# Kernel tuning notes

Hardware: AMD Instinct MI355X
Metric: run time of the kernel (lower is better)

Reference implementation:

```python
import jax, jax.numpy as jnp
import numpy as np

B, C, H, W = 32, 256, 64, 64
HEADS, KDIM, VDIM = 8, 64, 64


def setup_inputs() -> dict:
    key = jax.random.key(0)
    ks = jax.random.split(key, 9)
    s = lambda fan: 1.0 / np.sqrt(fan)
    x = jax.random.normal(ks[0], (B, C, H, W), jnp.float32)
    Wq = jax.random.normal(ks[1], (KDIM * HEADS, C), jnp.float32) * s(C)
    bq = jnp.zeros((KDIM * HEADS,), jnp.float32)
    Wk = jax.random.normal(ks[2], (KDIM, C), jnp.float32) * s(C)
    bk = jnp.zeros((KDIM,), jnp.float32)
    Wv = jax.random.normal(ks[3], (VDIM, C), jnp.float32) * s(C)
    bv = jnp.zeros((VDIM,), jnp.float32)
    Wo = jax.random.normal(ks[4], (C, VDIM * HEADS), jnp.float32) * s(VDIM * HEADS)
    bo = jnp.zeros((C,), jnp.float32)
    return {"x": x, "Wq": Wq, "bq": bq, "Wk": Wk, "bk": bk,
            "Wv": Wv, "bv": bv, "Wo": Wo, "bo": bo}


def reference(x, Wq, bq, Wk, bk, Wv, bv, Wo, bo):
    b, c, h, w = x.shape
    n = h * w
    kd = Wk.shape[0]
    heads = Wq.shape[0] // kd
    xf = x.reshape(b, c, n)
    # 1x1 convs == channel matmuls
    q = jnp.einsum('oc,bcn->bon', Wq, xf) + bq[None, :, None]  # (b, heads*kd, n)
    k = jnp.einsum('oc,bcn->bon', Wk, xf) + bk[None, :, None]  # (b, kd, n)
    v = jnp.einsum('oc,bcn->bon', Wv, xf) + bv[None, :, None]  # (b, vd, n)
    q = q.reshape(b, heads, kd, n)
    q = jax.nn.softmax(q, axis=2)   # softmax over key_dim (dim=2 of bhdn)
    k = jax.nn.softmax(k, axis=2)   # softmax over n (dim=2 of bdn)
    ctx = jnp.einsum('bdn,ben->bde', k, v)          # (b, kd, vd)
    out = jnp.einsum('bhdn,bde->bhen', q, ctx)      # (b, heads, vd, n)
    out = out.reshape(b, heads * ctx.shape[2], n)
    out = jnp.einsum('oc,bcn->bon', Wo, out) + bo[None, :, None]
    return out.reshape(b, -1, h, w)
```

## Files before the change

kernel.cpp:

```cpp
#include <hip/hip_runtime.h>
#include <hip/hip_bf16.h>
#include <stdint.h>

#define BATCH 32
#define CDIM  256
#define NPIX  4096
#define HEADS 8
#define KD    64
#define VD    64
#define OQ    512

typedef __hip_bfloat16 bf16;
typedef __attribute__((ext_vector_type(8))) short bf16x8;
typedef __attribute__((ext_vector_type(4))) float floatx4;

union pack8 { bf16 h[8]; uint4 u; };

__device__ inline uint4 cvt8(const float* __restrict__ s) {
  float4 f0 = *reinterpret_cast<const float4*>(s);
  float4 f1 = *reinterpret_cast<const float4*>(s + 4);
  pack8 t;
  t.h[0] = __float2bfloat16(f0.x); t.h[1] = __float2bfloat16(f0.y);
  t.h[2] = __float2bfloat16(f0.z); t.h[3] = __float2bfloat16(f0.w);
  t.h[4] = __float2bfloat16(f1.x); t.h[5] = __float2bfloat16(f1.y);
  t.h[6] = __float2bfloat16(f1.z); t.h[7] = __float2bfloat16(f1.w);
  return t.u;
}

__global__ __launch_bounds__(256) void transpose_k(const float* __restrict__ x,
                                                   bf16* __restrict__ xT) {
  __shared__ bf16 t[64 * 72];
  const int tid = threadIdx.x;
  const int b = blockIdx.z;
  const int n0 = blockIdx.x * 64;
  const int c0 = blockIdx.y * 64;
  const float* xb = x + (size_t)b * CDIM * NPIX;
  for (int p = 0; p < 2; ++p) {
    int cl = p * 32 + (tid >> 3);
    int no = (tid & 7) * 8;
    *reinterpret_cast<uint4*>(&t[cl * 72 + no]) =
        cvt8(xb + (size_t)(c0 + cl) * NPIX + n0 + no);
  }
  __syncthreads();
  bf16* xTb = xT + (size_t)b * NPIX * CDIM;
  for (int p = 0; p < 2; ++p) {
    int nl = p * 32 + (tid >> 3);
    int co = (tid & 7) * 8;
    pack8 tmp;
    for (int j = 0; j < 8; ++j) tmp.h[j] = t[(co + j) * 72 + nl];
    *reinterpret_cast<uint4*>(xTb + (size_t)(n0 + nl) * CDIM + c0 + co) = tmp.u;
  }
}

__global__ __launch_bounds__(256, 2) void gemm_qkv(
    const bf16* __restrict__ xT,
    const float* __restrict__ Wq, const float* __restrict__ bq,
    const float* __restrict__ Wk, const float* __restrict__ bk,
    const float* __restrict__ Wv, const float* __restrict__ bv,
    bf16* __restrict__ qT, bf16* __restrict__ kT, bf16* __restrict__ vT) {
  __shared__ bf16 lsA[128 * 72];
  __shared__ bf16 lsB[128 * 72];
  const int tid = threadIdx.x;
  const int b  = blockIdx.z;
  const int bm = blockIdx.x;
  const int ot = blockIdx.y;
  const int lane = tid & 63;
  const int w    = tid >> 6;
  const int wm = w & 1, wn = w >> 1;
  const int l15 = lane & 15, quad = lane >> 4;

  const bf16* Ab = xT + (size_t)b * NPIX * CDIM + (size_t)bm * 128 * CDIM;

  floatx4 acc[4][4];
  const floatx4 zf = {0.f, 0.f, 0.f, 0.f};
  for (int i = 0; i < 4; ++i)
    for (int j = 0; j < 4; ++j) acc[i][j] = zf;

  for (int kb = 0; kb < CDIM / 64; ++kb) {
    __syncthreads();
    for (int ci = tid; ci < 1024; ci += 256) {
      int row = ci >> 3, off = (ci & 7) << 3;
      uint4 v = *reinterpret_cast<const uint4*>(Ab + (size_t)row * CDIM + kb * 64 + off);
      *reinterpret_cast<uint4*>(&lsA[row * 72 + off]) = v;
    }
    for (int ci = tid; ci < 1024; ci += 256) {
      int row = ci >> 3, off = (ci & 7) << 3;
      int o = ot * 128 + row;
      const float* src = (o < 512) ? (Wq + (size_t)o * CDIM)
                        : (o < 576) ? (Wk + (size_t)(o - 512) * CDIM)
                                    : (Wv + (size_t)(o - 576) * CDIM);
      *reinterpret_cast<uint4*>(&lsB[row * 72 + off]) = cvt8(src + kb * 64 + off);
    }
    __syncthreads();
    for (int kk = 0; kk < 64; kk += 32) {
      bf16x8 af[4], bfr[4];
      for (int mi = 0; mi < 4; ++mi)
        af[mi] = *reinterpret_cast<const bf16x8*>(&lsA[(wm * 64 + mi * 16 + l15) * 72 + kk + quad * 8]);
      for (int ni = 0; ni < 4; ++ni)
        bfr[ni] = *reinterpret_cast<const bf16x8*>(&lsB[(wn * 64 + ni * 16 + l15) * 72 + kk + quad * 8]);
      for (int mi = 0; mi < 4; ++mi)
        for (int ni = 0; ni < 4; ++ni)
          acc[mi][ni] = __builtin_amdgcn_mfma_f32_16x16x32_bf16(af[mi], bfr[ni], acc[mi][ni], 0, 0, 0);
    }
  }
  __syncthreads();

  bf16* ep = ((w < 2) ? lsA : lsB) + (w & 1) * (64 * 72);
  const int obase = ot * 128 + wn * 64;

  if (obase < 512) {
    float bias[4];
    for (int ni = 0; ni < 4; ++ni) bias[ni] = bq[obase + ni * 16 + l15];
    for (int mi = 0; mi < 4; ++mi) {
      for (int r = 0; r < 4; ++r) {
        float v0 = acc[mi][0][r] + bias[0];
        float v1 = acc[mi][1][r] + bias[1];
        float v2 = acc[mi][2][r] + bias[2];
        float v3 = acc[mi][3][r] + bias[3];
        float m = fmaxf(fmaxf(v0, v1), fmaxf(v2, v3));
        for (int off = 1; off < 16; off <<= 1) m = fmaxf(m, __shfl_xor(m, off));
        float e0 = __expf(v0 - m), e1 = __expf(v1 - m);
        float e2 = __expf(v2 - m), e3 = __expf(v3 - m);
        float s = e0 + e1 + e2 + e3;
        for (int off = 1; off < 16; off <<= 1) s += __shfl_xor(s, off);
        float inv = 1.0f / s;
        int lr = mi * 16 + quad * 4 + r;
        ep[lr * 72 +  0 + l15] = __float2bfloat16(e0 * inv);
        ep[lr * 72 + 16 + l15] = __float2bfloat16(e1 * inv);
        ep[lr * 72 + 32 + l15] = __float2bfloat16(e2 * inv);
        ep[lr * 72 + 48 + l15] = __float2bfloat16(e3 * inv);
      }
    }
  } else {
    const float* bp = (wn == 0) ? bk : bv;
    float bias[4];
    for (int ni = 0; ni < 4; ++ni) bias[ni] = bp[ni * 16 + l15];
    for (int mi = 0; mi < 4; ++mi)
      for (int r = 0; r < 4; ++r) {
        int lr = mi * 16 + quad * 4 + r;
        for (int ni = 0; ni < 4; ++ni)
          ep[lr * 72 + ni * 16 + l15] = __float2bfloat16(acc[mi][ni][r] + bias[ni]);
      }
  }
  __syncthreads();

  bf16* dst; int rstride;
  const int row0 = bm * 128 + wm * 64;
  if (obase < 512)      { dst = qT + (size_t)b * NPIX * OQ + (size_t)row0 * OQ + obase; rstride = OQ; }
  else if (obase == 512){ dst = kT + (size_t)b * NPIX * KD + (size_t)row0 * KD;         rstride = KD; }
  else                  { dst = vT + (size_t)b * NPIX * VD + (size_t)row0 * VD;         rstride = VD; }
  for (int p = 0; p < 8; ++p) {
    int lr = (lane >> 3) + p * 8;
    int co = (lane & 7) * 8;
    uint4 v = *reinterpret_cast<const uint4*>(&ep[lr * 72 + co]);
    *reinterpret_cast<uint4*>(dst + (size_t)lr * rstride + co) = v;
  }
}

__global__ __launch_bounds__(256) void ctx_partial(const bf16* __restrict__ kT,
                                                   const bf16* __restrict__ vT,
                                                   float* __restrict__ ctxn,
                                                   float* __restrict__ dnm) {
  __shared__ float ek[16 * 68];
  __shared__ float vv[16 * 68];
  const int tid = threadIdx.x;
  const int b = blockIdx.y, ci = blockIdx.x;
  const int dg = tid >> 4, eg = tid & 15;
  float acc[4][4] = {};
  float dloc = 0.f;
  for (int nb = 0; nb < 16; ++nb) {
    const int n0 = ci * 256 + nb * 16;
    __syncthreads();
    if (tid < 128) {
      int r = tid >> 3, off = (tid & 7) * 8;
      const bf16* src = kT + (size_t)b * NPIX * KD + (size_t)(n0 + r) * KD + off;
      for (int j = 0; j < 8; ++j) ek[r * 68 + off + j] = __expf(__bfloat162float(src[j]));
    } else {
      int t2 = tid - 128;
      int r = t2 >> 3, off = (t2 & 7) * 8;
      const bf16* src = vT + (size_t)b * NPIX * VD + (size_t)(n0 + r) * VD + off;
      for (int j = 0; j < 8; ++j) vv[r * 68 + off + j] = __bfloat162float(src[j]);
    }
    __syncthreads();
    for (int nn = 0; nn < 16; ++nn) {
      float4 e4 = *reinterpret_cast<const float4*>(&ek[nn * 68 + dg * 4]);
      float4 v4 = *reinterpret_cast<const float4*>(&vv[nn * 68 + eg * 4]);
      acc[0][0] += e4.x * v4.x; acc[0][1] += e4.x * v4.y; acc[0][2] += e4.x * v4.z; acc[0][3] += e4.x * v4.w;
      acc[1][0] += e4.y * v4.x; acc[1][1] += e4.y * v4.y; acc[1][2] += e4.y * v4.z; acc[1][3] += e4.y * v4.w;
      acc[2][0] += e4.z * v4.x; acc[2][1] += e4.z * v4.y; acc[2][2] += e4.z * v4.z; acc[2][3] += e4.z * v4.w;
      acc[3][0] += e4.w * v4.x; acc[3][1] += e4.w * v4.y; acc[3][2] += e4.w * v4.z; acc[3][3] += e4.w * v4.w;
    }
    if (tid < 64) {
      for (int nn = 0; nn < 16; ++nn) dloc += ek[nn * 68 + tid];
    }
  }
  for (int i = 0; i < 4; ++i)
    for (int j = 0; j < 4; ++j)
      atomicAdd(&ctxn[(size_t)b * 4096 + (dg * 4 + i) * 64 + eg * 4 + j], acc[i][j]);
  if (tid < 64) atomicAdd(&dnm[b * 64 + tid], dloc);
}

__global__ __launch_bounds__(256) void mbuild(const float* __restrict__ ctxn,
                                              const float* __restrict__ dnm,
                                              const float* __restrict__ Wo,
                                              bf16* __restrict__ Mm) {
  __shared__ float cn[64 * 68];
  const int h = blockIdx.x, b = blockIdx.y, tid = threadIdx.x;
  for (int ii = tid; ii < 4096; ii += 256) {
    int d = ii >> 6;
    cn[d * 68 + (ii & 63)] = ctxn[(size_t)b * 4096 + ii] / dnm[b * 64 + d];
  }
  __syncthreads();
  const int c = tid;
  const float* wrow = Wo + (size_t)c * OQ + h * 64;
  float wv[64];
  for (int e = 0; e < 64; ++e) wv[e] = wrow[e];
  bf16* mrow = Mm + (size_t)b * CDIM * OQ + (size_t)c * OQ + h * 64;
  for (int d = 0; d < 64; ++d) {
    float a = 0.f;
    for (int e = 0; e < 64; ++e) a += wv[e] * cn[d * 68 + e];
    mrow[d] = __float2bfloat16(a);
  }
}

__global__ __launch_bounds__(256, 2) void gemm_out(
    const bf16* __restrict__ Mm, const bf16* __restrict__ qT,
    const float* __restrict__ bo, float* __restrict__ out) {
  __shared__ bf16 lsA[128 * 72];
  __shared__ bf16 lsB[128 * 72];
  const int tid = threadIdx.x;
  const int b  = blockIdx.z;
  const int cm = blockIdx.x;
  const int nt = blockIdx.y;
  const int lane = tid & 63;
  const int w    = tid >> 6;
  const int wm = w & 1, wn = w >> 1;
  const int l15 = lane & 15, quad = lane >> 4;

  const bf16* Ab = Mm + (size_t)b * CDIM * OQ + (size_t)cm * 128 * OQ;
  const bf16* Bb = qT + (size_t)b * NPIX * OQ + (size_t)nt * 128 * OQ;

  floatx4 acc[4][4];
  const floatx4 zf = {0.f, 0.f, 0.f, 0.f};
  for (int i = 0; i < 4; ++i)
    for (int j = 0; j < 4; ++j) acc[i][j] = zf;

  for (int kb = 0; kb < OQ / 64; ++kb) {
    __syncthreads();
    for (int ci = tid; ci < 1024; ci += 256) {
      int row = ci >> 3, off = (ci & 7) << 3;
      uint4 v = *reinterpret_cast<const uint4*>(Ab + (size_t)row * OQ + kb * 64 + off);
      *reinterpret_cast<uint4*>(&lsA[row * 72 + off]) = v;
    }
    for (int ci = tid; ci < 1024; ci += 256) {
      int row = ci >> 3, off = (ci & 7) << 3;
      uint4 v = *reinterpret_cast<const uint4*>(Bb + (size_t)row * OQ + kb * 64 + off);
      *reinterpret_cast<uint4*>(&lsB[row * 72 + off]) = v;
    }
    __syncthreads();
    for (int kk = 0; kk < 64; kk += 32) {
      bf16x8 af[4], bfr[4];
      for (int mi = 0; mi < 4; ++mi)
        af[mi] = *reinterpret_cast<const bf16x8*>(&lsA[(wm * 64 + mi * 16 + l15) * 72 + kk + quad * 8]);
      for (int ni = 0; ni < 4; ++ni)
        bfr[ni] = *reinterpret_cast<const bf16x8*>(&lsB[(wn * 64 + ni * 16 + l15) * 72 + kk + quad * 8]);
      for (int mi = 0; mi < 4; ++mi)
        for (int ni = 0; ni < 4; ++ni)
          acc[mi][ni] = __builtin_amdgcn_mfma_f32_16x16x32_bf16(af[mi], bfr[ni], acc[mi][ni], 0, 0, 0);
    }
  }

  const int row0 = cm * 128 + wm * 64;
  const int col0 = nt * 128 + wn * 64;
  float* outb = out + (size_t)b * CDIM * NPIX;
  for (int mi = 0; mi < 4; ++mi)
    for (int r = 0; r < 4; ++r) {
      int c = row0 + mi * 16 + quad * 4 + r;
      float bias = bo[c];
      float* orow = outb + (size_t)c * NPIX + col0;
      for (int ni = 0; ni < 4; ++ni)
        orow[ni * 16 + l15] = acc[mi][ni][r] + bias;
    }
}

extern "C" void kernel_launch(void* const* d_in, const int* in_sizes, int n_in,
                              void* d_out, int out_size, void* d_ws, size_t ws_size,
                              hipStream_t stream) {
  const float* x  = (const float*)d_in[0];
  const float* Wq = (const float*)d_in[1];
  const float* bq = (const float*)d_in[2];
  const float* Wk = (const float*)d_in[3];
  const float* bk = (const float*)d_in[4];
  const float* Wv = (const float*)d_in[5];
  const float* bv = (const float*)d_in[6];
  const float* Wo = (const float*)d_in[7];
  const float* bo = (const float*)d_in[8];
  float* out = (float*)d_out;

  const size_t pb_xT  = (size_t)NPIX * CDIM * 2;
  const size_t pb_qT  = (size_t)NPIX * OQ * 2;
  const size_t pb_kT  = (size_t)NPIX * KD * 2;
  const size_t pb_vT  = (size_t)NPIX * VD * 2;
  const size_t pb_ctx = (size_t)KD * VD * 4;
  const size_t pb_dnm = (size_t)KD * 4;
  const size_t pb_Mm  = (size_t)CDIM * OQ * 2;
  const size_t perB = pb_xT + pb_qT + pb_kT + pb_vT + pb_ctx + pb_dnm + pb_Mm;

  int CB = 32;
  while (CB > 1 && (size_t)CB * perB > ws_size) CB >>= 1;

  char* ws = (char*)d_ws;
  bf16*  xT   = (bf16*)ws;                                  ws += (size_t)CB * pb_xT;
  bf16*  qT   = (bf16*)ws;                                  ws += (size_t)CB * pb_qT;
  bf16*  kT   = (bf16*)ws;                                  ws += (size_t)CB * pb_kT;
  bf16*  vT   = (bf16*)ws;                                  ws += (size_t)CB * pb_vT;
  float* ctxn = (float*)ws;                                 ws += (size_t)CB * pb_ctx;
  float* dnm  = (float*)ws;                                 ws += (size_t)CB * pb_dnm;
  bf16*  Mm   = (bf16*)ws;

  for (int b0 = 0; b0 < BATCH; b0 += CB) {
    const float* x_c  = x   + (size_t)b0 * CDIM * NPIX;
    float*      out_c = out + (size_t)b0 * CDIM * NPIX;
    hipMemsetAsync(ctxn, 0, (size_t)CB * (pb_ctx + pb_dnm), stream);
    transpose_k<<<dim3(64, 4, CB), 256, 0, stream>>>(x_c, xT);
    gemm_qkv<<<dim3(32, 5, CB), 256, 0, stream>>>(xT, Wq, bq, Wk, bk, Wv, bv, qT, kT, vT);
    ctx_partial<<<dim3(16, CB), 256, 0, stream>>>(kT, vT, ctxn, dnm);
    mbuild<<<dim3(HEADS, CB), 256, 0, stream>>>(ctxn, dnm, Wo, Mm);
    gemm_out<<<dim3(2, 32, CB), 256, 0, stream>>>(Mm, qT, bo, out_c);
  }
}
```

Measured before the change: 533.5 us.

## Use direct global-to-LDS loads with XOR-swizzled tiles and pre-converted bf16 weights

Both MFMA GEMMs now stage their tiles with global_load_lds 16-byte transfers straight into LDS, in place of register round-trips. The padded layout is replaced by an unpadded one with an XOR swizzle to avoid bank conflicts. The QKV weights are converted to bf16 once, in a new prep kernel, instead of every block converting fp32 weights on each K-step. The swizzled layout adds index arithmetic and depends on the async LDS-load semantics being correct.

```diff
diff --git a/kernel.cpp b/kernel.cpp
--- a/kernel.cpp
+++ b/kernel.cpp
@@ -9,6 +9,7 @@
 #define KD    64
 #define VD    64
 #define OQ    512
+#define OTOT  640
 
 typedef __hip_bfloat16 bf16;
 typedef __attribute__((ext_vector_type(8))) short bf16x8;
@@ -25,6 +26,34 @@
   t.h[4] = __float2bfloat16(f1.x); t.h[5] = __float2bfloat16(f1.y);
   t.h[6] = __float2bfloat16(f1.z); t.h[7] = __float2bfloat16(f1.w);
   return t.u;
+}
+
+__device__ inline void gload16(const bf16* g, bf16* l) {
+  __builtin_amdgcn_global_load_lds(
+      (const __attribute__((address_space(1))) void*)(g),
+      (__attribute__((address_space(3))) void*)(l), 16, 0, 0);
+}
+
+__device__ inline bf16x8 lds_frag(const bf16* base, int row, int colbyte) {
+  int off = row * 128 + (colbyte ^ ((row & 7) << 4));
+  return *reinterpret_cast<const bf16x8*>(reinterpret_cast<const char*>(base) + off);
+}
+__device__ inline void ep_store(bf16* ep, int row, int colbyte, bf16 v) {
+  int off = row * 128 + (colbyte ^ ((row & 7) << 4));
+  *reinterpret_cast<bf16*>(reinterpret_cast<char*>(ep) + off) = v;
+}
+
+__global__ __launch_bounds__(256) void prep_w(const float* __restrict__ Wq,
+                                              const float* __restrict__ Wk,
+                                              const float* __restrict__ Wv,
+                                              bf16* __restrict__ Wb) {
+  int i = blockIdx.x * 256 + threadIdx.x;
+  int o = i >> 5;
+  int off = (i & 31) * 8;
+  const float* src = (o < OQ)      ? (Wq + (size_t)o * CDIM + off)
+                   : (o < OQ + KD) ? (Wk + (size_t)(o - OQ) * CDIM + off)
+                                   : (Wv + (size_t)(o - OQ - KD) * CDIM + off);
+  *reinterpret_cast<uint4*>(Wb + (size_t)o * CDIM + off) = cvt8(src);
 }
 
 __global__ __launch_bounds__(256) void transpose_k(const float* __restrict__ x,
@@ -53,13 +82,12 @@
 }
 
 __global__ __launch_bounds__(256, 2) void gemm_qkv(
-    const bf16* __restrict__ xT,
-    const float* __restrict__ Wq, const float* __restrict__ bq,
-    const float* __restrict__ Wk, const float* __restrict__ bk,
-    const float* __restrict__ Wv, const float* __restrict__ bv,
+    const bf16* __restrict__ xT, const bf16* __restrict__ Wb,
+    const float* __restrict__ bq, const float* __restrict__ bk,
+    const float* __restrict__ bv,
     bf16* __restrict__ qT, bf16* __restrict__ kT, bf16* __restrict__ vT) {
-  __shared__ bf16 lsA[128 * 72];
-  __shared__ bf16 lsB[128 * 72];
+  __shared__ bf16 lsA[128 * 64];
+  __shared__ bf16 lsB[128 * 64];
   const int tid = threadIdx.x;
   const int b  = blockIdx.z;
   const int bm = blockIdx.x;
@@ -70,6 +98,10 @@
   const int l15 = lane & 15, quad = lane >> 4;
 
   const bf16* Ab = xT + (size_t)b * NPIX * CDIM + (size_t)bm * 128 * CDIM;
+  const bf16* Bb = Wb + (size_t)ot * 128 * CDIM;
+
+  const int sr = lane >> 3;
+  const int sc = lane & 7;
 
   floatx4 acc[4][4];
   const floatx4 zf = {0.f, 0.f, 0.f, 0.f};
@@ -78,26 +110,21 @@
 
   for (int kb = 0; kb < CDIM / 64; ++kb) {
     __syncthreads();
-    for (int ci = tid; ci < 1024; ci += 256) {
-      int row = ci >> 3, off = (ci & 7) << 3;
-      uint4 v = *reinterpret_cast<const uint4*>(Ab + (size_t)row * CDIM + kb * 64 + off);
-      *reinterpret_cast<uint4*>(&lsA[row * 72 + off]) = v;
-    }
-    for (int ci = tid; ci < 1024; ci += 256) {
-      int row = ci >> 3, off = (ci & 7) << 3;
-      int o = ot * 128 + row;
-      const float* src = (o < 512) ? (Wq + (size_t)o * CDIM)
-                        : (o < 576) ? (Wk + (size_t)(o - 512) * CDIM)
-                                    : (Wv + (size_t)(o - 576) * CDIM);
-      *reinterpret_cast<uint4*>(&lsB[row * 72 + off]) = cvt8(src + kb * 64 + off);
-    }
-    __syncthreads();
+#pragma unroll
+    for (int it = 0; it < 4; ++it) {
+      const int r = w * 32 + it * 8 + sr;
+      const int c16 = sc ^ (r & 7);
+      gload16(Ab + (size_t)r * CDIM + kb * 64 + c16 * 8, &lsA[(w * 4 + it) * 512]);
+      gload16(Bb + (size_t)r * CDIM + kb * 64 + c16 * 8, &lsB[(w * 4 + it) * 512]);
+    }
+    __syncthreads();
+#pragma unroll
     for (int kk = 0; kk < 64; kk += 32) {
       bf16x8 af[4], bfr[4];
       for (int mi = 0; mi < 4; ++mi)
-        af[mi] = *reinterpret_cast<const bf16x8*>(&lsA[(wm * 64 + mi * 16 + l15) * 72 + kk + quad * 8]);
+        af[mi] = lds_frag(lsA, wm * 64 + mi * 16 + l15, kk * 2 + quad * 16);
       for (int ni = 0; ni < 4; ++ni)
-        bfr[ni] = *reinterpret_cast<const bf16x8*>(&lsB[(wn * 64 + ni * 16 + l15) * 72 + kk + quad * 8]);
+        bfr[ni] = lds_frag(lsB, wn * 64 + ni * 16 + l15, kk * 2 + quad * 16);
       for (int mi = 0; mi < 4; ++mi)
         for (int ni = 0; ni < 4; ++ni)
           acc[mi][ni] = __builtin_amdgcn_mfma_f32_16x16x32_bf16(af[mi], bfr[ni], acc[mi][ni], 0, 0, 0);
@@ -105,7 +132,7 @@
   }
   __syncthreads();
 
-  bf16* ep = ((w < 2) ? lsA : lsB) + (w & 1) * (64 * 72);
+  bf16* ep = ((w < 2) ? lsA : lsB) + (w & 1) * (64 * 64);
   const int obase = ot * 128 + wn * 64;
 
   if (obase < 512) {
@@ -125,10 +152,10 @@
         for (int off = 1; off < 16; off <<= 1) s += __shfl_xor(s, off);
         float inv = 1.0f / s;
         int lr = mi * 16 + quad * 4 + r;
-        ep[lr * 72 +  0 + l15] = __float2bfloat16(e0 * inv);
-        ep[lr * 72 + 16 + l15] = __float2bfloat16(e1 * inv);
-        ep[lr * 72 + 32 + l15] = __float2bfloat16(e2 * inv);
-        ep[lr * 72 + 48 + l15] = __float2bfloat16(e3 * inv);
+        ep_store(ep, lr, ( 0 + l15) * 2, __float2bfloat16(e0 * inv));
+        ep_store(ep, lr, (16 + l15) * 2, __float2bfloat16(e1 * inv));
+        ep_store(ep, lr, (32 + l15) * 2, __float2bfloat16(e2 * inv));
+        ep_store(ep, lr, (48 + l15) * 2, __float2bfloat16(e3 * inv));
       }
     }
   } else {
@@ -139,7 +166,8 @@
       for (int r = 0; r < 4; ++r) {
         int lr = mi * 16 + quad * 4 + r;
         for (int ni = 0; ni < 4; ++ni)
-          ep[lr * 72 + ni * 16 + l15] = __float2bfloat16(acc[mi][ni][r] + bias[ni]);
+          ep_store(ep, lr, (ni * 16 + l15) * 2,
+                   __float2bfloat16(acc[mi][ni][r] + bias[ni]));
       }
   }
   __syncthreads();
@@ -151,9 +179,10 @@
   else                  { dst = vT + (size_t)b * NPIX * VD + (size_t)row0 * VD;         rstride = VD; }
   for (int p = 0; p < 8; ++p) {
     int lr = (lane >> 3) + p * 8;
-    int co = (lane & 7) * 8;
-    uint4 v = *reinterpret_cast<const uint4*>(&ep[lr * 72 + co]);
-    *reinterpret_cast<uint4*>(dst + (size_t)lr * rstride + co) = v;
+    int cb = (lane & 7) * 16;
+    int off = lr * 128 + (cb ^ ((lr & 7) << 4));
+    uint4 v = *reinterpret_cast<const uint4*>(reinterpret_cast<const char*>(ep) + off);
+    *reinterpret_cast<uint4*>(dst + (size_t)lr * rstride + (cb >> 1)) = v;
   }
 }
 
@@ -226,8 +255,8 @@
 __global__ __launch_bounds__(256, 2) void gemm_out(
     const bf16* __restrict__ Mm, const bf16* __restrict__ qT,
     const float* __restrict__ bo, float* __restrict__ out) {
-  __shared__ bf16 lsA[128 * 72];
-  __shared__ bf16 lsB[128 * 72];
+  __shared__ bf16 lsA[128 * 64];
+  __shared__ bf16 lsB[128 * 64];
   const int tid = threadIdx.x;
   const int b  = blockIdx.z;
   const int cm = blockIdx.x;
@@ -240,6 +269,9 @@
   const bf16* Ab = Mm + (size_t)b * CDIM * OQ + (size_t)cm * 128 * OQ;
   const bf16* Bb = qT + (size_t)b * NPIX * OQ + (size_t)nt * 128 * OQ;
 
+  const int sr = lane >> 3;
+  const int sc = lane & 7;
+
   floatx4 acc[4][4];
   const floatx4 zf = {0.f, 0.f, 0.f, 0.f};
   for (int i = 0; i < 4; ++i)
@@ -247,23 +279,21 @@
 
   for (int kb = 0; kb < OQ / 64; ++kb) {
     __syncthreads();
-    for (int ci = tid; ci < 1024; ci += 256) {
-      int row = ci >> 3, off = (ci & 7) << 3;
-      uint4 v = *reinterpret_cast<const uint4*>(Ab + (size_t)row * OQ + kb * 64 + off);
-      *reinterpret_cast<uint4*>(&lsA[row * 72 + off]) = v;
-    }
-    for (int ci = tid; ci < 1024; ci += 256) {
-      int row = ci >> 3, off = (ci & 7) << 3;
-      uint4 v = *reinterpret_cast<const uint4*>(Bb + (size_t)row * OQ + kb * 64 + off);
-      *reinterpret_cast<uint4*>(&lsB[row * 72 + off]) = v;
-    }
-    __syncthreads();
+#pragma unroll
+    for (int it = 0; it < 4; ++it) {
+      const int r = w * 32 + it * 8 + sr;
+      const int c16 = sc ^ (r & 7);
+      gload16(Ab + (size_t)r * OQ + kb * 64 + c16 * 8, &lsA[(w * 4 + it) * 512]);
+      gload16(Bb + (size_t)r * OQ + kb * 64 + c16 * 8, &lsB[(w * 4 + it) * 512]);
+    }
+    __syncthreads();
+#pragma unroll
     for (int kk = 0; kk < 64; kk += 32) {
       bf16x8 af[4], bfr[4];
       for (int mi = 0; mi < 4; ++mi)
-        af[mi] = *reinterpret_cast<const bf16x8*>(&lsA[(wm * 64 + mi * 16 + l15) * 72 + kk + quad * 8]);
+        af[mi] = lds_frag(lsA, wm * 64 + mi * 16 + l15, kk * 2 + quad * 16);
       for (int ni = 0; ni < 4; ++ni)
-        bfr[ni] = *reinterpret_cast<const bf16x8*>(&lsB[(wn * 64 + ni * 16 + l15) * 72 + kk + quad * 8]);
+        bfr[ni] = lds_frag(lsB, wn * 64 + ni * 16 + l15, kk * 2 + quad * 16);
       for (int mi = 0; mi < 4; ++mi)
         for (int ni = 0; ni < 4; ++ni)
           acc[mi][ni] = __builtin_amdgcn_mfma_f32_16x16x32_bf16(af[mi], bfr[ni], acc[mi][ni], 0, 0, 0);
@@ -297,6 +327,7 @@
   const float* bo = (const float*)d_in[8];
   float* out = (float*)d_out;
 
+  const size_t pb_W   = (size_t)OTOT * CDIM * 2;
   const size_t pb_xT  = (size_t)NPIX * CDIM * 2;
   const size_t pb_qT  = (size_t)NPIX * OQ * 2;
   const size_t pb_kT  = (size_t)NPIX * KD * 2;
@@ -307,9 +338,10 @@
   const size_t perB = pb_xT + pb_qT + pb_kT + pb_vT + pb_ctx + pb_dnm + pb_Mm;
 
   int CB = 32;
-  while (CB > 1 && (size_t)CB * perB > ws_size) CB >>= 1;
+  while (CB > 1 && (size_t)CB * perB + pb_W > ws_size) CB >>= 1;
 
   char* ws = (char*)d_ws;
+  bf16*  Wb   = (bf16*)ws;                                  ws += pb_W;
   bf16*  xT   = (bf16*)ws;                                  ws += (size_t)CB * pb_xT;
   bf16*  qT   = (bf16*)ws;                                  ws += (size_t)CB * pb_qT;
   bf16*  kT   = (bf16*)ws;                                  ws += (size_t)CB * pb_kT;
@@ -318,12 +350,14 @@
   float* dnm  = (float*)ws;                                 ws += (size_t)CB * pb_dnm;
   bf16*  Mm   = (bf16*)ws;
 
+  prep_w<<<dim3(80), 256, 0, stream>>>(Wq, Wk, Wv, Wb);
+
   for (int b0 = 0; b0 < BATCH; b0 += CB) {
     const float* x_c  = x   + (size_t)b0 * CDIM * NPIX;
     float*      out_c = out + (size_t)b0 * CDIM * NPIX;
     hipMemsetAsync(ctxn, 0, (size_t)CB * (pb_ctx + pb_dnm), stream);
     transpose_k<<<dim3(64, 4, CB), 256, 0, stream>>>(x_c, xT);
-    gemm_qkv<<<dim3(32, 5, CB), 256, 0, stream>>>(xT, Wq, bq, Wk, bk, Wv, bv, qT, kT, vT);
+    gemm_qkv<<<dim3(32, 5, CB), 256, 0, stream>>>(xT, Wb, bq, bk, bv, qT, kT, vT);
     ctx_partial<<<dim3(16, CB), 256, 0, stream>>>(kT, vT, ctxn, dnm);
     mbuild<<<dim3(HEADS, CB), 256, 0, stream>>>(ctxn, dnm, Wo, Mm);
     gemm_out<<<dim3(2, 32, CB), 256, 0, stream>>>(Mm, qT, bo, out_c);
```

Result: faster. 484.4 us (-9.2%).
